# Kernel tuning notes

Hardware: AMD Instinct MI355X
Metric: run time of the kernel (lower is better)

The kernel has to match this reference:

```python
import jax, jax.numpy as jnp
import numpy as np

B, T, C = 2, 2048, 768
NH = 12
HS = C // NH


def setup_inputs() -> dict:
    key = jax.random.key(0)
    k1, k2, k3 = jax.random.split(key, 3)
    x = jax.random.normal(k1, (B, T, C), dtype=jnp.float32)
    # c_attn: Linear(C, 3C). Stored as (C, 3C) so y = x @ w + b (same math as torch x @ W.T + b).
    w_attn = jax.random.normal(k2, (C, 3 * C), dtype=jnp.float32) * (1.0 / np.sqrt(C))
    b_attn = jax.random.normal(k3, (3 * C,), dtype=jnp.float32) * 0.02
    return {"x": x, "w_attn": w_attn, "b_attn": b_attn}


def reference(x, w_attn, b_attn):
    b, t, c = x.shape
    qkv = x @ w_attn + b_attn                      # [B, T, 3C]
    q, k, v = jnp.split(qkv, 3, axis=-1)
    # [B, T, C] -> [B, NH, T, HS]
    q = q.reshape(b, t, NH, HS).transpose(0, 2, 1, 3)
    k = k.reshape(b, t, NH, HS).transpose(0, 2, 1, 3)
    v = v.reshape(b, t, NH, HS).transpose(0, 2, 1, 3)
    scale = 1.0 / np.sqrt(HS).astype(np.float32)
    wei = jnp.einsum("bhqd,bhkd->bhqk", q, k) * scale   # [B, NH, T, T]
    causal = jnp.tril(jnp.ones((t, t), dtype=bool))
    wei = jnp.where(causal[None, None, :, :], wei, -jnp.inf)
    wei = jax.nn.softmax(wei, axis=-1)
    out = jnp.einsum("bhqk,bhkd->bhqd", wei, v)          # [B, NH, T, HS]
    # NOTE: original module returns here, before head-merge / output projection.
    return out
```

## Files before the change

### kernel.cpp

```cpp
#include <hip/hip_runtime.h>

typedef __bf16 bf16_t;
typedef __bf16 bf16x8 __attribute__((ext_vector_type(8)));
typedef __bf16 bf16x4 __attribute__((ext_vector_type(4)));
typedef _Float16 f16x4 __attribute__((ext_vector_type(4)));
typedef _Float16 f16x8 __attribute__((ext_vector_type(8)));
typedef float f32x4 __attribute__((ext_vector_type(4)));

#define B_   2
#define T_   2048
#define C_   768
#define NH_  12
#define HS_  64
#define N3_  2304
#define M_   4096

__device__ __forceinline__ bf16_t f2bf(float f) {
  unsigned u = __builtin_bit_cast(unsigned, f);
  u += 0x7fffu + ((u >> 16) & 1u);
  unsigned short s = (unsigned short)(u >> 16);
  return __builtin_bit_cast(bf16_t, s);
}

__global__ __launch_bounds__(256) void cvt_xw_kernel(const float* __restrict__ x,
                                                     const float* __restrict__ w,
                                                     bf16_t* __restrict__ xb,
                                                     bf16_t* __restrict__ wt) {
  __shared__ float tile[32][33];
  int bx = blockIdx.x;
  if (bx < 3072) {
    int i = (bx * 256 + threadIdx.x) * 4;
    float4 v = *reinterpret_cast<const float4*>(x + i);
    xb[i + 0] = f2bf(v.x);
    xb[i + 1] = f2bf(v.y);
    xb[i + 2] = f2bf(v.z);
    xb[i + 3] = f2bf(v.w);
  } else {
    int b = bx - 3072;
    int k0 = (b % 24) * 32, n0 = (b / 24) * 32;
    int tx = threadIdx.x & 31, ty = threadIdx.x >> 5;
#pragma unroll
    for (int i = 0; i < 4; i++)
      tile[ty + i * 8][tx] = w[(size_t)(k0 + ty + i * 8) * N3_ + n0 + tx];
    __syncthreads();
#pragma unroll
    for (int i = 0; i < 4; i++)
      wt[(size_t)(n0 + ty + i * 8) * C_ + k0 + tx] = f2bf(tile[tx][ty + i * 8]);
  }
}

__global__ __launch_bounds__(256) void gemm_qkv(const bf16_t* __restrict__ xb,
                                                const bf16_t* __restrict__ wt,
                                                const float* __restrict__ bias,
                                                bf16_t* __restrict__ qout,
                                                bf16_t* __restrict__ kout,
                                                _Float16* __restrict__ va) {
  __shared__ bf16_t As[128 * 32];
  __shared__ bf16_t Bs[128 * 32];
  const int tid = threadIdx.x;
  const int lane = tid & 63, wave = tid >> 6;
  const int wm = wave >> 1, wn = wave & 1;
  const int quad = lane >> 4, l15 = lane & 15;
  const int row0 = blockIdx.y * 128;
  const int col0 = blockIdx.x * 128;
  const bool isqk = (col0 < 1536);

  f32x4 acc[4][4];
#pragma unroll
  for (int mi = 0; mi < 4; mi++)
#pragma unroll
    for (int ni = 0; ni < 4; ni++) acc[mi][ni] = f32x4{0.f, 0.f, 0.f, 0.f};

  for (int k0 = 0; k0 < C_; k0 += 32) {
#pragma unroll
    for (int c = 0; c < 2; c++) {
      int chunk = c * 256 + tid;
      int r = chunk >> 2, qd = chunk & 3;
      const bf16_t* ga = xb + (size_t)(row0 + r) * C_ + k0 + qd * 8;
      const bf16_t* gb = wt + (size_t)(col0 + r) * C_ + k0 + qd * 8;
      char* la = (char*)As + (size_t)(c * 256 + wave * 64) * 16;
      char* lb = (char*)Bs + (size_t)(c * 256 + wave * 64) * 16;
      __builtin_amdgcn_global_load_lds((const __attribute__((address_space(1))) void*)ga,
                                       (__attribute__((address_space(3))) void*)la, 16, 0, 0);
      __builtin_amdgcn_global_load_lds((const __attribute__((address_space(1))) void*)gb,
                                       (__attribute__((address_space(3))) void*)lb, 16, 0, 0);
    }
    __syncthreads();

    bf16x8 af[4], bfr[4];
#pragma unroll
    for (int mi = 0; mi < 4; mi++)
      af[mi] = *reinterpret_cast<const bf16x8*>(&As[(wm * 64 + mi * 16 + l15) * 32 + quad * 8]);
#pragma unroll
    for (int ni = 0; ni < 4; ni++)
      bfr[ni] = *reinterpret_cast<const bf16x8*>(&Bs[(wn * 64 + ni * 16 + l15) * 32 + quad * 8]);
    if (isqk) {
#pragma unroll
      for (int mi = 0; mi < 4; mi++)
#pragma unroll
        for (int ni = 0; ni < 4; ni++)
          acc[mi][ni] = __builtin_amdgcn_mfma_f32_16x16x32_bf16(bfr[ni], af[mi], acc[mi][ni], 0, 0, 0);
    } else {
#pragma unroll
      for (int mi = 0; mi < 4; mi++)
#pragma unroll
        for (int ni = 0; ni < 4; ni++)
          acc[mi][ni] = __builtin_amdgcn_mfma_f32_16x16x32_bf16(af[mi], bfr[ni], acc[mi][ni], 0, 0, 0);
    }
    __syncthreads();
  }

  if (isqk) {
#pragma unroll
    for (int mi = 0; mi < 4; mi++) {
      int t = row0 + wm * 64 + mi * 16 + l15;
      int b = t >> 11, tt = t & 2047;
#pragma unroll
      for (int ni = 0; ni < 4; ni++) {
        int cN0 = col0 + wn * 64 + ni * 16 + quad * 4;
        int which = cN0 / 768;
        int rem = cN0 - which * 768;
        int h = rem >> 6, d0 = rem & 63;
        float4 bv = *reinterpret_cast<const float4*>(bias + cN0);
        bf16x4 pack;
        pack[0] = f2bf(acc[mi][ni][0] + bv.x);
        pack[1] = f2bf(acc[mi][ni][1] + bv.y);
        pack[2] = f2bf(acc[mi][ni][2] + bv.z);
        pack[3] = f2bf(acc[mi][ni][3] + bv.w);
        bf16_t* dst = which ? kout : qout;
        *reinterpret_cast<bf16x4*>(dst + (((size_t)b * NH_ + h) * T_ + tt) * HS_ + d0) = pack;
      }
    }
  } else {
#pragma unroll
    for (int mi = 0; mi < 4; mi++) {
      int trow = row0 + wm * 64 + mi * 16 + quad * 4;
      int b = trow >> 11, tt = trow & 2047;
      int kt = tt >> 6, nj = (tt >> 4) & 3, qd = (tt >> 2) & 3;
#pragma unroll
      for (int ni = 0; ni < 4; ni++) {
        int cN = col0 + wn * 64 + ni * 16 + l15;
        int rem = cN - 1536;
        int h = rem >> 6, d = rem & 63;
        int bh = b * NH_ + h;
        float bv = bias[cN];
        f16x4 pk;
#pragma unroll
        for (int r = 0; r < 4; r++) pk[r] = (_Float16)(acc[mi][ni][r] + bv);
        size_t off = ((((((size_t)bh * 32 + kt) * 4 + nj) * 4 + qd) * 16 + (d & 15)) * 16) + (d >> 4) * 4;
        *reinterpret_cast<f16x4*>(va + off) = pk;
      }
    }
  }
}

__global__ __launch_bounds__(256) void attn_kernel(const bf16_t* __restrict__ qb,
                                                   const bf16_t* __restrict__ kb,
                                                   const _Float16* __restrict__ va,
                                                   float* __restrict__ out) {
  __shared__ bf16_t Ks[2][64][72];
  __shared__ _Float16 Vs[2][4][2][64][8];
  const int tid = threadIdx.x;
  const int lane = tid & 63, wave = tid >> 6;
  const int quad = lane >> 4, l15 = lane & 15;
  const int pairIdx = (int)blockIdx.x;
  const int bh = (int)blockIdx.z * NH_ + (int)blockIdx.y;
  const bf16_t* Qg = qb + (size_t)bh * T_ * HS_;
  const bf16_t* Kg = kb + (size_t)bh * T_ * HS_;
  const _Float16* Vg = va + (size_t)bh * 32 * 4096;

  const int krow = tid >> 2, kcol = (tid & 3) * 16;
  const int vni = tid >> 6, vlane = tid & 63;

  int4 rk0, rk1, rv0, rv1;
  auto GLOAD = [&](int kt) {
    const char* kp = (const char*)(Kg + (size_t)kt * 64 * HS_) + krow * 128 + kcol * 2;
    rk0 = *reinterpret_cast<const int4*>(kp);
    rk1 = *reinterpret_cast<const int4*>(kp + 16);
    const char* vp = (const char*)(Vg + (size_t)kt * 4096) + tid * 32;
    rv0 = *reinterpret_cast<const int4*>(vp);
    rv1 = *reinterpret_cast<const int4*>(vp + 16);
  };
  auto SSTORE = [&](int buf) {
    char* kd = (char*)&Ks[buf][krow][kcol];
    *reinterpret_cast<int4*>(kd) = rk0;
    *reinterpret_cast<int4*>(kd + 16) = rk1;
    *reinterpret_cast<int4*>(&Vs[buf][vni][0][vlane][0]) = rv0;
    *reinterpret_cast<int4*>(&Vs[buf][vni][1][vlane][0]) = rv1;
  };

#pragma unroll
  for (int part = 0; part < 2; part++) {
    const int qtile = part ? pairIdx : 31 - pairIdx;
    const int qrow_base = qtile * 64 + wave * 16;
    const int qmax = qrow_base + 15;
    const int qcol = qrow_base + l15;
    const int nkt = qtile + 1;

    bf16x8 bq0 = *reinterpret_cast<const bf16x8*>(Qg + (size_t)qcol * HS_ + quad * 8);
    bf16x8 bq1 = *reinterpret_cast<const bf16x8*>(Qg + (size_t)qcol * HS_ + 32 + quad * 8);

    float lsum = 0.f;
    f32x4 Oacc[4];
#pragma unroll
    for (int mi = 0; mi < 4; mi++) Oacc[mi] = f32x4{0.f, 0.f, 0.f, 0.f};

    GLOAD(0);
    __syncthreads();
    SSTORE(0);
    __syncthreads();

    for (int kt = 0; kt < nkt; kt++) {
      const int cur = kt & 1;
      const bool last = (kt + 1 >= nkt);
      if (!last) GLOAD(kt + 1);

      const bool diag = (kt == nkt - 1);
      f16x4 pf[4];
#pragma unroll
      for (int ni = 0; ni < 4; ni++) {
        if (diag && (kt * 64 + ni * 16 > qmax)) continue;
        bf16x8 ka0 = *reinterpret_cast<const bf16x8*>(&Ks[cur][ni * 16 + l15][quad * 8]);
        bf16x8 ka1 = *reinterpret_cast<const bf16x8*>(&Ks[cur][ni * 16 + l15][32 + quad * 8]);
        f32x4 s = {0.f, 0.f, 0.f, 0.f};
        s = __builtin_amdgcn_mfma_f32_16x16x32_bf16(ka0, bq0, s, 0, 0, 0);
        s = __builtin_amdgcn_mfma_f32_16x16x32_bf16(ka1, bq1, s, 0, 0, 0);
#pragma unroll
        for (int r = 0; r < 4; r++) {
          float p = __expf(s[r] * 0.125f);
          if (diag) {
            int j = kt * 64 + ni * 16 + quad * 4 + r;
            if (j > qcol) p = 0.f;
          }
          lsum += p;
          pf[ni][r] = (_Float16)p;
        }
      }
#pragma unroll
      for (int ni = 0; ni < 4; ni++) {
        if (diag && (kt * 64 + ni * 16 > qmax)) continue;
#pragma unroll
        for (int p = 0; p < 2; p++) {
          f16x8 vv = *reinterpret_cast<const f16x8*>(&Vs[cur][ni][p][lane][0]);
          f16x4 lo = __builtin_shufflevector(vv, vv, 0, 1, 2, 3);
          f16x4 hi = __builtin_shufflevector(vv, vv, 4, 5, 6, 7);
          Oacc[2 * p]     = __builtin_amdgcn_mfma_f32_16x16x16f16(lo, pf[ni], Oacc[2 * p], 0, 0, 0);
          Oacc[2 * p + 1] = __builtin_amdgcn_mfma_f32_16x16x16f16(hi, pf[ni], Oacc[2 * p + 1], 0, 0, 0);
        }
      }

      if (!last) {
        SSTORE(1 - cur);
        __syncthreads();
      }
    }

    lsum += __shfl_xor(lsum, 16, 64);
    lsum += __shfl_xor(lsum, 32, 64);
    float rinv = 1.0f / lsum;

#pragma unroll
    for (int mi = 0; mi < 4; mi++) {
      float4 o;
      o.x = Oacc[mi][0] * rinv;
      o.y = Oacc[mi][1] * rinv;
      o.z = Oacc[mi][2] * rinv;
      o.w = Oacc[mi][3] * rinv;
      *reinterpret_cast<float4*>(out + ((size_t)bh * T_ + qcol) * HS_ + mi * 16 + quad * 4) = o;
    }
  }
}

extern "C" void kernel_launch(void* const* d_in, const int* in_sizes, int n_in,
                              void* d_out, int out_size, void* d_ws, size_t ws_size,
                              hipStream_t stream) {
  const float* x = (const float*)d_in[0];
  const float* w = (const float*)d_in[1];
  const float* bias = (const float*)d_in[2];
  float* out = (float*)d_out;

  char* ws = (char*)d_ws;
  bf16_t* xb = (bf16_t*)(ws);
  bf16_t* wt = (bf16_t*)(ws + 6291456);
  bf16_t* qb = (bf16_t*)(ws + 6291456 + 3538944);
  bf16_t* kb = qb + 3145728;
  _Float16* va = (_Float16*)(kb + 3145728);

  cvt_xw_kernel<<<dim3(3072 + 1728), dim3(256), 0, stream>>>(x, w, xb, wt);
  gemm_qkv<<<dim3(N3_ / 128, M_ / 128), dim3(256), 0, stream>>>(xb, wt, bias, qb, kb, va);
  attn_kernel<<<dim3(16, NH_, B_), dim3(256), 0, stream>>>(qb, kb, va, out);
}
```

Measured before the change: 152.1 us.

## Split attention key range across two blocks and combine partial sums

```diff
diff --git a/kernel.cpp b/kernel.cpp
--- a/kernel.cpp
+++ b/kernel.cpp
@@ -14,6 +14,8 @@
 #define HS_  64
 #define N3_  2304
 #define M_   4096
+#define NOUT 3145728
+#define NQ   49152
 
 __device__ __forceinline__ bf16_t f2bf(float f) {
   unsigned u = __builtin_bit_cast(unsigned, f);
@@ -157,13 +159,15 @@
 __global__ __launch_bounds__(256) void attn_kernel(const bf16_t* __restrict__ qb,
                                                    const bf16_t* __restrict__ kb,
                                                    const _Float16* __restrict__ va,
-                                                   float* __restrict__ out) {
+                                                   float* __restrict__ opart,
+                                                   float* __restrict__ lpart) {
   __shared__ bf16_t Ks[2][64][72];
   __shared__ _Float16 Vs[2][4][2][64][8];
   const int tid = threadIdx.x;
   const int lane = tid & 63, wave = tid >> 6;
   const int quad = lane >> 4, l15 = lane & 15;
-  const int pairIdx = (int)blockIdx.x;
+  const int pairIdx = (int)blockIdx.x >> 1;
+  const int half = (int)blockIdx.x & 1;
   const int bh = (int)blockIdx.z * NH_ + (int)blockIdx.y;
   const bf16_t* Qg = qb + (size_t)bh * T_ * HS_;
   const bf16_t* Kg = kb + (size_t)bh * T_ * HS_;
@@ -196,6 +200,9 @@
     const int qmax = qrow_base + 15;
     const int qcol = qrow_base + l15;
     const int nkt = qtile + 1;
+    const int khalf = (nkt + 1) >> 1;
+    const int kt0 = half ? khalf : 0;
+    const int kt1 = half ? nkt : khalf;
 
     bf16x8 bq0 = *reinterpret_cast<const bf16x8*>(Qg + (size_t)qcol * HS_ + quad * 8);
     bf16x8 bq1 = *reinterpret_cast<const bf16x8*>(Qg + (size_t)qcol * HS_ + 32 + quad * 8);
@@ -205,70 +212,81 @@
 #pragma unroll
     for (int mi = 0; mi < 4; mi++) Oacc[mi] = f32x4{0.f, 0.f, 0.f, 0.f};
 
-    GLOAD(0);
-    __syncthreads();
-    SSTORE(0);
-    __syncthreads();
-
-    for (int kt = 0; kt < nkt; kt++) {
-      const int cur = kt & 1;
-      const bool last = (kt + 1 >= nkt);
-      if (!last) GLOAD(kt + 1);
-
-      const bool diag = (kt == nkt - 1);
-      f16x4 pf[4];
-#pragma unroll
-      for (int ni = 0; ni < 4; ni++) {
-        if (diag && (kt * 64 + ni * 16 > qmax)) continue;
-        bf16x8 ka0 = *reinterpret_cast<const bf16x8*>(&Ks[cur][ni * 16 + l15][quad * 8]);
-        bf16x8 ka1 = *reinterpret_cast<const bf16x8*>(&Ks[cur][ni * 16 + l15][32 + quad * 8]);
-        f32x4 s = {0.f, 0.f, 0.f, 0.f};
-        s = __builtin_amdgcn_mfma_f32_16x16x32_bf16(ka0, bq0, s, 0, 0, 0);
-        s = __builtin_amdgcn_mfma_f32_16x16x32_bf16(ka1, bq1, s, 0, 0, 0);
-#pragma unroll
-        for (int r = 0; r < 4; r++) {
-          float p = __expf(s[r] * 0.125f);
-          if (diag) {
-            int j = kt * 64 + ni * 16 + quad * 4 + r;
-            if (j > qcol) p = 0.f;
+    if (kt1 > kt0) {
+      GLOAD(kt0);
+      __syncthreads();
+      SSTORE(0);
+      __syncthreads();
+
+      for (int kt = kt0; kt < kt1; kt++) {
+        const int cur = (kt - kt0) & 1;
+        const bool last = (kt + 1 >= kt1);
+        if (!last) GLOAD(kt + 1);
+
+        const bool diag = (kt == nkt - 1);
+        f16x4 pf[4];
+#pragma unroll
+        for (int ni = 0; ni < 4; ni++) {
+          if (diag && (kt * 64 + ni * 16 > qmax)) continue;
+          bf16x8 ka0 = *reinterpret_cast<const bf16x8*>(&Ks[cur][ni * 16 + l15][quad * 8]);
+          bf16x8 ka1 = *reinterpret_cast<const bf16x8*>(&Ks[cur][ni * 16 + l15][32 + quad * 8]);
+          f32x4 s = {0.f, 0.f, 0.f, 0.f};
+          s = __builtin_amdgcn_mfma_f32_16x16x32_bf16(ka0, bq0, s, 0, 0, 0);
+          s = __builtin_amdgcn_mfma_f32_16x16x32_bf16(ka1, bq1, s, 0, 0, 0);
+#pragma unroll
+          for (int r = 0; r < 4; r++) {
+            float p = __builtin_amdgcn_exp2f(s[r] * 0.18033688011112042f);
+            if (diag) {
+              int j = kt * 64 + ni * 16 + quad * 4 + r;
+              if (j > qcol) p = 0.f;
+            }
+            lsum += p;
+            pf[ni][r] = (_Float16)p;
           }
-          lsum += p;
-          pf[ni][r] = (_Float16)p;
+        }
+#pragma unroll
+        for (int ni = 0; ni < 4; ni++) {
+          if (diag && (kt * 64 + ni * 16 > qmax)) continue;
+#pragma unroll
+          for (int p = 0; p < 2; p++) {
+            f16x8 vv = *reinterpret_cast<const f16x8*>(&Vs[cur][ni][p][lane][0]);
+            f16x4 lo = __builtin_shufflevector(vv, vv, 0, 1, 2, 3);
+            f16x4 hi = __builtin_shufflevector(vv, vv, 4, 5, 6, 7);
+            Oacc[2 * p]     = __builtin_amdgcn_mfma_f32_16x16x16f16(lo, pf[ni], Oacc[2 * p], 0, 0, 0);
+            Oacc[2 * p + 1] = __builtin_amdgcn_mfma_f32_16x16x16f16(hi, pf[ni], Oacc[2 * p + 1], 0, 0, 0);
+          }
+        }
+
+        if (!last) {
+          SSTORE(1 - cur);
+          __syncthreads();
         }
       }
-#pragma unroll
-      for (int ni = 0; ni < 4; ni++) {
-        if (diag && (kt * 64 + ni * 16 > qmax)) continue;
-#pragma unroll
-        for (int p = 0; p < 2; p++) {
-          f16x8 vv = *reinterpret_cast<const f16x8*>(&Vs[cur][ni][p][lane][0]);
-          f16x4 lo = __builtin_shufflevector(vv, vv, 0, 1, 2, 3);
-          f16x4 hi = __builtin_shufflevector(vv, vv, 4, 5, 6, 7);
-          Oacc[2 * p]     = __builtin_amdgcn_mfma_f32_16x16x16f16(lo, pf[ni], Oacc[2 * p], 0, 0, 0);
-          Oacc[2 * p + 1] = __builtin_amdgcn_mfma_f32_16x16x16f16(hi, pf[ni], Oacc[2 * p + 1], 0, 0, 0);
-        }
-      }
-
-      if (!last) {
-        SSTORE(1 - cur);
-        __syncthreads();
-      }
     }
 
     lsum += __shfl_xor(lsum, 16, 64);
     lsum += __shfl_xor(lsum, 32, 64);
-    float rinv = 1.0f / lsum;
-
-#pragma unroll
-    for (int mi = 0; mi < 4; mi++) {
-      float4 o;
-      o.x = Oacc[mi][0] * rinv;
-      o.y = Oacc[mi][1] * rinv;
-      o.z = Oacc[mi][2] * rinv;
-      o.w = Oacc[mi][3] * rinv;
-      *reinterpret_cast<float4*>(out + ((size_t)bh * T_ + qcol) * HS_ + mi * 16 + quad * 4) = o;
-    }
+
+    float* Op = opart + (size_t)half * NOUT + ((size_t)bh * T_ + qcol) * HS_;
+#pragma unroll
+    for (int mi = 0; mi < 4; mi++)
+      *reinterpret_cast<f32x4*>(Op + mi * 16 + quad * 4) = Oacc[mi];
+    if (lane < 16)
+      lpart[(size_t)half * NQ + (size_t)bh * T_ + qrow_base + l15] = lsum;
   }
+}
+
+__global__ __launch_bounds__(256) void attn_combine(const float* __restrict__ opart,
+                                                    const float* __restrict__ lpart,
+                                                    float* __restrict__ out) {
+  const int idx = blockIdx.x * 256 + threadIdx.x;
+  const int base = idx * 4;
+  const int q = idx >> 4;
+  f32x4 a = *reinterpret_cast<const f32x4*>(opart + base);
+  f32x4 b = *reinterpret_cast<const f32x4*>(opart + NOUT + base);
+  float rinv = 1.0f / (lpart[q] + lpart[NQ + q]);
+  f32x4 o = (a + b) * rinv;
+  *reinterpret_cast<f32x4*>(out + base) = o;
 }
 
 extern "C" void kernel_launch(void* const* d_in, const int* in_sizes, int n_in,
@@ -285,8 +303,11 @@
   bf16_t* qb = (bf16_t*)(ws + 6291456 + 3538944);
   bf16_t* kb = qb + 3145728;
   _Float16* va = (_Float16*)(kb + 3145728);
+  float* opart = (float*)((char*)va + 6291456);
+  float* lpart = opart + 2 * NOUT;
 
   cvt_xw_kernel<<<dim3(3072 + 1728), dim3(256), 0, stream>>>(x, w, xb, wt);
   gemm_qkv<<<dim3(N3_ / 128, M_ / 128), dim3(256), 0, stream>>>(xb, wt, bias, qb, kb, va);
-  attn_kernel<<<dim3(16, NH_, B_), dim3(256), 0, stream>>>(qb, kb, va, out);
-}
+  attn_kernel<<<dim3(32, NH_, B_), dim3(256), 0, stream>>>(qb, kb, va, opart, lpart);
+  attn_combine<<<dim3(NOUT / 1024), dim3(256), 0, stream>>>(opart, lpart, out);
+}
```

New measurement: 157.3 us. +3.4%, slower.
